# Optimization experiments

Measured on AMD Instinct MI355X. Metric: run time of the kernel, lower is better.

## Reference

```python
import jax, jax.numpy as jnp
import numpy as np

N_NODES = 50000
N_EDGES = 800000
N_GRAPHS = 256
D_IN, D_H1, D_H2, D_OUT = 64, 64, 64, 64


def gcn_conv(x, W, b, src, dst, n_nodes):
    # PyG GCNConv (eval): h = x @ W; add self-loops; deg[i] = in_deg(i) + 1;
    # out[i] = sum_{j->i} h[j] * deg[i]^-1/2 deg[j]^-1/2 + h[i]/deg[i] + b
    h = x @ W  # [N, F]
    ones = jnp.ones((src.shape[0],), dtype=x.dtype)
    deg = jax.ops.segment_sum(ones, dst, num_segments=n_nodes) + 1.0  # self loop
    dinv = jax.lax.rsqrt(deg)
    norm = dinv[src] * dinv[dst]  # [E]
    msg = h[src] * norm[:, None]  # [E, F]  (memory-bound gather)
    agg = jax.ops.segment_sum(msg, dst, num_segments=n_nodes)  # scatter-add
    agg = agg + h * (1.0 / deg)[:, None]  # self-loop contribution
    return agg + b


def setup_inputs() -> dict:
    key = jax.random.key(0)
    ks = jax.random.split(key, 12)
    x = jax.random.normal(ks[0], (N_NODES, D_IN), dtype=jnp.float32)
    src = jax.random.randint(ks[1], (N_EDGES,), 0, N_NODES)
    dst = jax.random.randint(ks[2], (N_EDGES,), 0, N_NODES)
    batch = jnp.sort(jax.random.randint(ks[3], (N_NODES,), 0, N_GRAPHS))
    def glorot(k, fin, fout):
        s = jnp.sqrt(6.0 / (fin + fout))
        return jax.random.uniform(k, (fin, fout), jnp.float32, -s, s)
    return {
        "x": x, "src": src, "dst": dst, "batch": batch,
        "W1": glorot(ks[4], D_IN, D_H1), "b1": jnp.zeros((D_H1,), jnp.float32),
        "W2": glorot(ks[5], D_H1, D_H2), "b2": jnp.zeros((D_H2,), jnp.float32),
        "W3": glorot(ks[6], D_H2, D_OUT), "b3": jnp.zeros((D_OUT,), jnp.float32),
        "Wl": glorot(ks[7], D_OUT, 1), "bl": jnp.zeros((1,), jnp.float32),
    }


def reference(x, src, dst, batch, W1, b1, W2, b2, W3, b3, Wl, bl):
    n = x.shape[0]
    h = jax.nn.relu(gcn_conv(x, W1, b1, src, dst, n))   # dropout inactive (eval)
    h = jax.nn.relu(gcn_conv(h, W2, b2, src, dst, n))
    h = jax.nn.relu(gcn_conv(h, W3, b3, src, dst, n))
    # global_mean_pool over graph ids
    sums = jax.ops.segment_sum(h, batch, num_segments=N_GRAPHS)  # [G, F]
    cnt = jax.ops.segment_sum(jnp.ones((n,), h.dtype), batch, num_segments=N_GRAPHS)
    pooled = sums / jnp.maximum(cnt, 1.0)[:, None]
    return pooled @ Wl + bl  # [G, 1]
```

## Files before the change

### kernel.cpp

```cpp
#include <hip/hip_runtime.h>

#define N_NODES 50000
#define N_EDGES 800000
#define N_GRAPHS 256
#define F 64
#define NBUCK 196
#define CAP 4608
#define P3_TILE 2048
#define P3_GRID ((N_EDGES + P3_TILE - 1) / P3_TILE)
#define BCAP 6144

__device__ __forceinline__ unsigned short f2bf(float f) {
    union { float f; unsigned u; } c; c.f = f;
    unsigned u = c.u + 0x7FFFu + ((c.u >> 16) & 1u);
    return (unsigned short)(u >> 16);
}
__device__ __forceinline__ float bfl(unsigned u) {
    union { unsigned u; float f; } c; c.u = u << 16; return c.f;
}
__device__ __forceinline__ float bfh(unsigned u) {
    union { unsigned u; float f; } c; c.u = u & 0xFFFF0000u; return c.f;
}

__global__ __launch_bounds__(256) void partition_edges(const int* __restrict__ src,
                                                       const int* __restrict__ dst,
                                                       int* __restrict__ bcur,
                                                       unsigned int* __restrict__ bpair) {
    __shared__ int bh[NBUCK], bloc[NBUCK], bpos[NBUCK];
    int t = threadIdx.x;
    int lo = blockIdx.x * P3_TILE;
    int hi = min(lo + P3_TILE, N_EDGES);
    for (int i = t; i < NBUCK; i += 256) { bh[i] = 0; bpos[i] = 0; }
    __syncthreads();
    for (int e = lo + t; e < hi; e += 256) atomicAdd(&bh[dst[e] >> 8], 1);
    __syncthreads();
    for (int i = t; i < NBUCK; i += 256)
        bloc[i] = bh[i] ? atomicAdd(&bcur[i], bh[i]) : 0;
    __syncthreads();
    for (int e = lo + t; e < hi; e += 256) {
        int d = dst[e];
        int b = d >> 8;
        int r = atomicAdd(&bpos[b], 1);
        bpair[(size_t)b * CAP + bloc[b] + r] = ((unsigned)src[e] << 8) | (unsigned)(d & 255);
    }
}

__global__ __launch_bounds__(256) void bucket_sort(const unsigned int* __restrict__ bpair,
                                                   const int* __restrict__ bcur,
                                                   int* __restrict__ eidx,
                                                   int* __restrict__ rbeg,
                                                   int* __restrict__ rend,
                                                   float* __restrict__ dinv) {
    __shared__ int cnt[256], s[256], pos[256];
    __shared__ int lout[BCAP];
    int b = blockIdx.x, t = threadIdx.x;
    int base = b * CAP;
    int sz = bcur[b];

    cnt[t] = 0;
    __syncthreads();
    for (int i = t; i < sz; i += 256) atomicAdd(&cnt[bpair[base + i] & 255], 1);
    __syncthreads();
    int v = cnt[t];
    s[t] = v;
    __syncthreads();
    for (int off = 1; off < 256; off <<= 1) {
        int u = (t >= off) ? s[t - off] : 0;
        __syncthreads();
        s[t] += u;
        __syncthreads();
    }
    int excl = s[t] - v;
    pos[t] = excl;
    int node = b * 256 + t;
    if (node < N_NODES) {
        rbeg[node] = base + excl;
        rend[node] = base + excl + v;
        dinv[node] = 1.0f / sqrtf((float)v + 1.0f);
    }
    __syncthreads();

    if (sz <= BCAP) {
        for (int i = t; i < sz; i += 256) {
            unsigned p = bpair[base + i];
            int r = atomicAdd(&pos[p & 255], 1);
            lout[r] = (int)((p >> 8) << 7);
        }
        __syncthreads();
        for (int i = t; i < sz; i += 256) eidx[base + i] = lout[i];
    } else {
        for (int i = t; i < sz; i += 256) {
            unsigned p = bpair[base + i];
            int r = atomicAdd(&pos[p & 255], 1);
            eidx[base + r] = (int)((p >> 8) << 7);
        }
    }
}

#define XSTRIDE 17
__global__ __launch_bounds__(256) void gemm64_v(const float* __restrict__ X,
                                                const float* __restrict__ W,
                                                const float* __restrict__ dinv,
                                                unsigned short* __restrict__ Hn, int n) {
    __shared__ float4 sW[64 * 16];
    __shared__ float4 sX[128 * XSTRIDE];
    int tid = threadIdx.x;
    int base = blockIdx.x * 128;

    const float4* W4 = (const float4*)W;
    for (int i = tid; i < 64 * 16; i += 256) sW[i] = W4[i];
    const float4* X4 = (const float4*)X;
    for (int i = tid; i < 128 * 16; i += 256) {
        int r = i >> 4, kg = i & 15;
        int node = base + r;
        sX[r * XSTRIDE + kg] = (node < n) ? X4[(size_t)node * 16 + kg]
                                          : make_float4(0.f, 0.f, 0.f, 0.f);
    }
    __syncthreads();

    int fg = tid & 15;
    int ng = tid >> 4;
    float4 acc[8];
#pragma unroll
    for (int ii = 0; ii < 8; ii++) acc[ii] = make_float4(0.f, 0.f, 0.f, 0.f);

    for (int kg = 0; kg < 16; kg++) {
        float4 xv[8];
#pragma unroll
        for (int ii = 0; ii < 8; ii++) xv[ii] = sX[(ng + 16 * ii) * XSTRIDE + kg];
#pragma unroll
        for (int kk = 0; kk < 4; kk++) {
            float4 wv = sW[(4 * kg + kk) * 16 + fg];
#pragma unroll
            for (int ii = 0; ii < 8; ii++) {
                float xs = (kk == 0) ? xv[ii].x : (kk == 1) ? xv[ii].y
                         : (kk == 2) ? xv[ii].z : xv[ii].w;
                acc[ii].x += wv.x * xs;
                acc[ii].y += wv.y * xs;
                acc[ii].z += wv.z * xs;
                acc[ii].w += wv.w * xs;
            }
        }
    }

    ushort4* H4 = (ushort4*)Hn;
#pragma unroll
    for (int ii = 0; ii < 8; ii++) {
        int node = base + ng + 16 * ii;
        if (node < n) {
            float d = dinv[node];
            float4 o = acc[ii];
            ushort4 u;
            u.x = f2bf(o.x * d); u.y = f2bf(o.y * d);
            u.z = f2bf(o.z * d); u.w = f2bf(o.w * d);
            H4[(size_t)node * 16 + fg] = u;
        }
    }
}

__global__ __launch_bounds__(256) void gather_layer(const int* __restrict__ rbeg,
                                                    const int* __restrict__ rend,
                                                    const int* __restrict__ eidx,
                                                    const float* __restrict__ dinv,
                                                    const unsigned short* __restrict__ Hn,
                                                    const float* __restrict__ b,
                                                    float* __restrict__ OUT, int n) {
    int w = (blockIdx.x * blockDim.x + threadIdx.x) >> 6;
    int lane = threadIdx.x & 63;
    if (w >= n) return;
    int g = lane >> 3;
    int f = lane & 7;
    int beg = rbeg[w], end = rend[w];
    const char* Hb = (const char*)Hn;

    float a0 = 0.f, a1 = 0.f, a2 = 0.f, a3 = 0.f;
    float a4 = 0.f, a5 = 0.f, a6 = 0.f, a7 = 0.f;
    int k = beg + g;
    for (; k + 8 < end; k += 16) {
        int o1 = eidx[k];
        int o2 = eidx[k + 8];
        uint4 p = *(const uint4*)(Hb + o1 + f * 16);
        uint4 q = *(const uint4*)(Hb + o2 + f * 16);
        a0 += bfl(p.x) + bfl(q.x); a1 += bfh(p.x) + bfh(q.x);
        a2 += bfl(p.y) + bfl(q.y); a3 += bfh(p.y) + bfh(q.y);
        a4 += bfl(p.z) + bfl(q.z); a5 += bfh(p.z) + bfh(q.z);
        a6 += bfl(p.w) + bfl(q.w); a7 += bfh(p.w) + bfh(q.w);
    }
    if (k < end) {
        int o1 = eidx[k];
        uint4 p = *(const uint4*)(Hb + o1 + f * 16);
        a0 += bfl(p.x); a1 += bfh(p.x);
        a2 += bfl(p.y); a3 += bfh(p.y);
        a4 += bfl(p.z); a5 += bfh(p.z);
        a6 += bfl(p.w); a7 += bfh(p.w);
    }
#pragma unroll
    for (int m = 8; m <= 32; m <<= 1) {
        a0 += __shfl_xor(a0, m); a1 += __shfl_xor(a1, m);
        a2 += __shfl_xor(a2, m); a3 += __shfl_xor(a3, m);
        a4 += __shfl_xor(a4, m); a5 += __shfl_xor(a5, m);
        a6 += __shfl_xor(a6, m); a7 += __shfl_xor(a7, m);
    }

    if (g == 0) {
        float di = dinv[w];
        uint4 hs = *(const uint4*)(Hb + (size_t)w * 128 + f * 16);
        float4 b0 = ((const float4*)b)[2 * f];
        float4 b1 = ((const float4*)b)[2 * f + 1];
        float4 o0, o1v;
        o0.x  = fmaxf(di * (a0 + bfl(hs.x)) + b0.x, 0.f);
        o0.y  = fmaxf(di * (a1 + bfh(hs.x)) + b0.y, 0.f);
        o0.z  = fmaxf(di * (a2 + bfl(hs.y)) + b0.z, 0.f);
        o0.w  = fmaxf(di * (a3 + bfh(hs.y)) + b0.w, 0.f);
        o1v.x = fmaxf(di * (a4 + bfl(hs.z)) + b1.x, 0.f);
        o1v.y = fmaxf(di * (a5 + bfh(hs.z)) + b1.y, 0.f);
        o1v.z = fmaxf(di * (a6 + bfl(hs.w)) + b1.z, 0.f);
        o1v.w = fmaxf(di * (a7 + bfh(hs.w)) + b1.w, 0.f);
        ((float4*)OUT)[(size_t)w * 16 + 2 * f]     = o0;
        ((float4*)OUT)[(size_t)w * 16 + 2 * f + 1] = o1v;
    }
}

__global__ __launch_bounds__(256) void gather_pool(const int* __restrict__ rbeg,
                                                   const int* __restrict__ rend,
                                                   const int* __restrict__ eidx,
                                                   const float* __restrict__ dinv,
                                                   const unsigned short* __restrict__ Hn,
                                                   const float* __restrict__ b,
                                                   const float* __restrict__ Wl,
                                                   float* __restrict__ pdot, int n) {
    int w = (blockIdx.x * blockDim.x + threadIdx.x) >> 6;
    int lane = threadIdx.x & 63;
    if (w >= n) return;
    int g = lane >> 3;
    int f = lane & 7;
    int beg = rbeg[w], end = rend[w];
    const char* Hb = (const char*)Hn;

    float a0 = 0.f, a1 = 0.f, a2 = 0.f, a3 = 0.f;
    float a4 = 0.f, a5 = 0.f, a6 = 0.f, a7 = 0.f;
    int k = beg + g;
    for (; k + 8 < end; k += 16) {
        int o1 = eidx[k];
        int o2 = eidx[k + 8];
        uint4 p = *(const uint4*)(Hb + o1 + f * 16);
        uint4 q = *(const uint4*)(Hb + o2 + f * 16);
        a0 += bfl(p.x) + bfl(q.x); a1 += bfh(p.x) + bfh(q.x);
        a2 += bfl(p.y) + bfl(q.y); a3 += bfh(p.y) + bfh(q.y);
        a4 += bfl(p.z) + bfl(q.z); a5 += bfh(p.z) + bfh(q.z);
        a6 += bfl(p.w) + bfl(q.w); a7 += bfh(p.w) + bfh(q.w);
    }
    if (k < end) {
        int o1 = eidx[k];
        uint4 p = *(const uint4*)(Hb + o1 + f * 16);
        a0 += bfl(p.x); a1 += bfh(p.x);
        a2 += bfl(p.y); a3 += bfh(p.y);
        a4 += bfl(p.z); a5 += bfh(p.z);
        a6 += bfl(p.w); a7 += bfh(p.w);
    }
#pragma unroll
    for (int m = 8; m <= 32; m <<= 1) {
        a0 += __shfl_xor(a0, m); a1 += __shfl_xor(a1, m);
        a2 += __shfl_xor(a2, m); a3 += __shfl_xor(a3, m);
        a4 += __shfl_xor(a4, m); a5 += __shfl_xor(a5, m);
        a6 += __shfl_xor(a6, m); a7 += __shfl_xor(a7, m);
    }

    float di = dinv[w];
    uint4 hs = *(const uint4*)(Hb + (size_t)w * 128 + f * 16);
    float4 b0 = ((const float4*)b)[2 * f];
    float4 b1 = ((const float4*)b)[2 * f + 1];
    float4 w0 = ((const float4*)Wl)[2 * f];
    float4 w1 = ((const float4*)Wl)[2 * f + 1];
    float d = 0.f;
    d += fmaxf(di * (a0 + bfl(hs.x)) + b0.x, 0.f) * w0.x;
    d += fmaxf(di * (a1 + bfh(hs.x)) + b0.y, 0.f) * w0.y;
    d += fmaxf(di * (a2 + bfl(hs.y)) + b0.z, 0.f) * w0.z;
    d += fmaxf(di * (a3 + bfh(hs.y)) + b0.w, 0.f) * w0.w;
    d += fmaxf(di * (a4 + bfl(hs.z)) + b1.x, 0.f) * w1.x;
    d += fmaxf(di * (a5 + bfh(hs.z)) + b1.y, 0.f) * w1.y;
    d += fmaxf(di * (a6 + bfl(hs.w)) + b1.z, 0.f) * w1.z;
    d += fmaxf(di * (a7 + bfh(hs.w)) + b1.w, 0.f) * w1.w;
#pragma unroll
    for (int m = 1; m <= 4; m <<= 1) d += __shfl_xor(d, m);
    if (lane == 0) pdot[w] = d;
}

__global__ __launch_bounds__(64) void final_out(const float* __restrict__ pdot,
                                                const int* __restrict__ batch,
                                                const float* __restrict__ bl,
                                                float* __restrict__ out) {
    int g = blockIdx.x;
    __shared__ int slo, shi;
    int lane = threadIdx.x;
    if (lane == 0) {
        int a = 0, b = N_NODES;
        while (a < b) { int m = (a + b) >> 1; if (batch[m] < g) a = m + 1; else b = m; }
        slo = a;
        b = N_NODES;
        while (a < b) { int m = (a + b) >> 1; if (batch[m] < g + 1) a = m + 1; else b = m; }
        shi = a;
    }
    __syncthreads();
    int lo = slo, hi = shi;
    float acc = 0.f;
    for (int i = lo + lane; i < hi; i += 64) acc += pdot[i];
#pragma unroll
    for (int off = 32; off > 0; off >>= 1) acc += __shfl_down(acc, off);
    if (lane == 0) {
        float cnt = (float)(hi - lo);
        out[g] = acc / fmaxf(cnt, 1.0f) + bl[0];
    }
}

extern "C" void kernel_launch(void* const* d_in, const int* in_sizes, int n_in,
                              void* d_out, int out_size, void* d_ws, size_t ws_size,
                              hipStream_t stream) {
    const float* x     = (const float*)d_in[0];
    const int*   src   = (const int*)d_in[1];
    const int*   dst   = (const int*)d_in[2];
    const int*   batch = (const int*)d_in[3];
    const float* W1 = (const float*)d_in[4];  const float* b1 = (const float*)d_in[5];
    const float* W2 = (const float*)d_in[6];  const float* b2 = (const float*)d_in[7];
    const float* W3 = (const float*)d_in[8];  const float* b3 = (const float*)d_in[9];
    const float* Wl = (const float*)d_in[10]; const float* bl = (const float*)d_in[11];
    float* out = (float*)d_out;

    char* ws = (char*)d_ws;
    unsigned short* Abf = (unsigned short*)ws;
    float* B       = (float*)(ws + (size_t)N_NODES * F * 2);
    float* dinv    = B + (size_t)N_NODES * F;
    float* pdot    = dinv + N_NODES;
    int*   rbeg    = (int*)(pdot + N_NODES);
    int*   rend    = rbeg + N_NODES;
    int*   bcur    = rend + N_NODES;
    unsigned int* bpair = (unsigned int*)(bcur + NBUCK);
    int*   eidx    = (int*)(bpair + (size_t)NBUCK * CAP);

    const int GEMM_GRID     = (N_NODES + 127) / 128;
    const int NODEWAVE_GRID = (N_NODES * 64 + 255) / 256;

    hipMemsetAsync(bcur, 0, NBUCK * sizeof(int), stream);
    partition_edges<<<P3_GRID, 256, 0, stream>>>(src, dst, bcur, bpair);
    bucket_sort<<<NBUCK, 256, 0, stream>>>(bpair, bcur, eidx, rbeg, rend, dinv);

    gemm64_v<<<GEMM_GRID, 256, 0, stream>>>(x, W1, dinv, Abf, N_NODES);
    gather_layer<<<NODEWAVE_GRID, 256, 0, stream>>>(rbeg, rend, eidx, dinv, Abf, b1, B, N_NODES);

    gemm64_v<<<GEMM_GRID, 256, 0, stream>>>(B, W2, dinv, Abf, N_NODES);
    gather_layer<<<NODEWAVE_GRID, 256, 0, stream>>>(rbeg, rend, eidx, dinv, Abf, b2, B, N_NODES);

    gemm64_v<<<GEMM_GRID, 256, 0, stream>>>(B, W3, dinv, Abf, N_NODES);
    gather_pool<<<NODEWAVE_GRID, 256, 0, stream>>>(rbeg, rend, eidx, dinv, Abf, b3, Wl, pdot, N_NODES);

    final_out<<<N_GRAPHS, 64, 0, stream>>>(pdot, batch, bl, out);
}
```

Measured before the change: 234.6 us.

## Store layer activations in bf16 and gather 8 nodes per wave

```diff
diff --git a/kernel.cpp b/kernel.cpp
--- a/kernel.cpp
+++ b/kernel.cpp
@@ -14,6 +14,9 @@
     union { float f; unsigned u; } c; c.f = f;
     unsigned u = c.u + 0x7FFFu + ((c.u >> 16) & 1u);
     return (unsigned short)(u >> 16);
+}
+__device__ __forceinline__ unsigned pack2bf(float lo, float hi) {
+    return (unsigned)f2bf(lo) | ((unsigned)f2bf(hi) << 16);
 }
 __device__ __forceinline__ float bfl(unsigned u) {
     union { unsigned u; float f; } c; c.u = u << 16; return c.f;
@@ -98,7 +101,8 @@
 }
 
 #define XSTRIDE 17
-__global__ __launch_bounds__(256) void gemm64_v(const float* __restrict__ X,
+template <bool BF16IN>
+__global__ __launch_bounds__(256) void gemm64_t(const void* __restrict__ Xv,
                                                 const float* __restrict__ W,
                                                 const float* __restrict__ dinv,
                                                 unsigned short* __restrict__ Hn, int n) {
@@ -109,12 +113,24 @@
 
     const float4* W4 = (const float4*)W;
     for (int i = tid; i < 64 * 16; i += 256) sW[i] = W4[i];
-    const float4* X4 = (const float4*)X;
-    for (int i = tid; i < 128 * 16; i += 256) {
-        int r = i >> 4, kg = i & 15;
-        int node = base + r;
-        sX[r * XSTRIDE + kg] = (node < n) ? X4[(size_t)node * 16 + kg]
-                                          : make_float4(0.f, 0.f, 0.f, 0.f);
+    if (BF16IN) {
+        const uint4* X4 = (const uint4*)Xv;
+        for (int i = tid; i < 128 * 8; i += 256) {
+            int r = i >> 3, c = i & 7;
+            int node = base + r;
+            uint4 u = (node < n) ? X4[(size_t)node * 8 + c]
+                                 : make_uint4(0u, 0u, 0u, 0u);
+            sX[r * XSTRIDE + 2 * c]     = make_float4(bfl(u.x), bfh(u.x), bfl(u.y), bfh(u.y));
+            sX[r * XSTRIDE + 2 * c + 1] = make_float4(bfl(u.z), bfh(u.z), bfl(u.w), bfh(u.w));
+        }
+    } else {
+        const float4* X4 = (const float4*)Xv;
+        for (int i = tid; i < 128 * 16; i += 256) {
+            int r = i >> 4, kg = i & 15;
+            int node = base + r;
+            sX[r * XSTRIDE + kg] = (node < n) ? X4[(size_t)node * 16 + kg]
+                                              : make_float4(0.f, 0.f, 0.f, 0.f);
+        }
     }
     __syncthreads();
 
@@ -164,21 +180,22 @@
                                                     const float* __restrict__ dinv,
                                                     const unsigned short* __restrict__ Hn,
                                                     const float* __restrict__ b,
-                                                    float* __restrict__ OUT, int n) {
-    int w = (blockIdx.x * blockDim.x + threadIdx.x) >> 6;
+                                                    unsigned short* __restrict__ OUT, int n) {
+    int wv = (blockIdx.x * blockDim.x + threadIdx.x) >> 6;
     int lane = threadIdx.x & 63;
-    if (w >= n) return;
-    int g = lane >> 3;
-    int f = lane & 7;
-    int beg = rbeg[w], end = rend[w];
+    int ns = lane >> 3, f = lane & 7;
+    int node = wv * 8 + ns;
+    bool valid = node < n;
+    int beg = valid ? rbeg[node] : 0;
+    int end = valid ? rend[node] : 0;
     const char* Hb = (const char*)Hn;
 
     float a0 = 0.f, a1 = 0.f, a2 = 0.f, a3 = 0.f;
     float a4 = 0.f, a5 = 0.f, a6 = 0.f, a7 = 0.f;
-    int k = beg + g;
-    for (; k + 8 < end; k += 16) {
+    int k = beg;
+    for (; k + 1 < end; k += 2) {
         int o1 = eidx[k];
-        int o2 = eidx[k + 8];
+        int o2 = eidx[k + 1];
         uint4 p = *(const uint4*)(Hb + o1 + f * 16);
         uint4 q = *(const uint4*)(Hb + o2 + f * 16);
         a0 += bfl(p.x) + bfl(q.x); a1 += bfh(p.x) + bfh(q.x);
@@ -194,30 +211,24 @@
         a4 += bfl(p.z); a5 += bfh(p.z);
         a6 += bfl(p.w); a7 += bfh(p.w);
     }
-#pragma unroll
-    for (int m = 8; m <= 32; m <<= 1) {
-        a0 += __shfl_xor(a0, m); a1 += __shfl_xor(a1, m);
-        a2 += __shfl_xor(a2, m); a3 += __shfl_xor(a3, m);
-        a4 += __shfl_xor(a4, m); a5 += __shfl_xor(a5, m);
-        a6 += __shfl_xor(a6, m); a7 += __shfl_xor(a7, m);
-    }
-
-    if (g == 0) {
-        float di = dinv[w];
-        uint4 hs = *(const uint4*)(Hb + (size_t)w * 128 + f * 16);
+
+    if (valid) {
+        float di = dinv[node];
+        uint4 hs = *(const uint4*)(Hb + (size_t)node * 128 + f * 16);
         float4 b0 = ((const float4*)b)[2 * f];
         float4 b1 = ((const float4*)b)[2 * f + 1];
-        float4 o0, o1v;
-        o0.x  = fmaxf(di * (a0 + bfl(hs.x)) + b0.x, 0.f);
-        o0.y  = fmaxf(di * (a1 + bfh(hs.x)) + b0.y, 0.f);
-        o0.z  = fmaxf(di * (a2 + bfl(hs.y)) + b0.z, 0.f);
-        o0.w  = fmaxf(di * (a3 + bfh(hs.y)) + b0.w, 0.f);
-        o1v.x = fmaxf(di * (a4 + bfl(hs.z)) + b1.x, 0.f);
-        o1v.y = fmaxf(di * (a5 + bfh(hs.z)) + b1.y, 0.f);
-        o1v.z = fmaxf(di * (a6 + bfl(hs.w)) + b1.z, 0.f);
-        o1v.w = fmaxf(di * (a7 + bfh(hs.w)) + b1.w, 0.f);
-        ((float4*)OUT)[(size_t)w * 16 + 2 * f]     = o0;
-        ((float4*)OUT)[(size_t)w * 16 + 2 * f + 1] = o1v;
+        float v0 = fmaxf(di * (a0 + bfl(hs.x)) + b0.x, 0.f);
+        float v1 = fmaxf(di * (a1 + bfh(hs.x)) + b0.y, 0.f);
+        float v2 = fmaxf(di * (a2 + bfl(hs.y)) + b0.z, 0.f);
+        float v3 = fmaxf(di * (a3 + bfh(hs.y)) + b0.w, 0.f);
+        float v4 = fmaxf(di * (a4 + bfl(hs.z)) + b1.x, 0.f);
+        float v5 = fmaxf(di * (a5 + bfh(hs.z)) + b1.y, 0.f);
+        float v6 = fmaxf(di * (a6 + bfl(hs.w)) + b1.z, 0.f);
+        float v7 = fmaxf(di * (a7 + bfh(hs.w)) + b1.w, 0.f);
+        uint4 u;
+        u.x = pack2bf(v0, v1); u.y = pack2bf(v2, v3);
+        u.z = pack2bf(v4, v5); u.w = pack2bf(v6, v7);
+        ((uint4*)OUT)[(size_t)node * 8 + f] = u;
     }
 }
 
@@ -229,20 +240,21 @@
                                                    const float* __restrict__ b,
                                                    const float* __restrict__ Wl,
                                                    float* __restrict__ pdot, int n) {
-    int w = (blockIdx.x * blockDim.x + threadIdx.x) >> 6;
+    int wv = (blockIdx.x * blockDim.x + threadIdx.x) >> 6;
     int lane = threadIdx.x & 63;
-    if (w >= n) return;
-    int g = lane >> 3;
-    int f = lane & 7;
-    int beg = rbeg[w], end = rend[w];
+    int ns = lane >> 3, f = lane & 7;
+    int node = wv * 8 + ns;
+    bool valid = node < n;
+    int beg = valid ? rbeg[node] : 0;
+    int end = valid ? rend[node] : 0;
     const char* Hb = (const char*)Hn;
 
     float a0 = 0.f, a1 = 0.f, a2 = 0.f, a3 = 0.f;
     float a4 = 0.f, a5 = 0.f, a6 = 0.f, a7 = 0.f;
-    int k = beg + g;
-    for (; k + 8 < end; k += 16) {
+    int k = beg;
+    for (; k + 1 < end; k += 2) {
         int o1 = eidx[k];
-        int o2 = eidx[k + 8];
+        int o2 = eidx[k + 1];
         uint4 p = *(const uint4*)(Hb + o1 + f * 16);
         uint4 q = *(const uint4*)(Hb + o2 + f * 16);
         a0 += bfl(p.x) + bfl(q.x); a1 += bfh(p.x) + bfh(q.x);
@@ -258,16 +270,10 @@
         a4 += bfl(p.z); a5 += bfh(p.z);
         a6 += bfl(p.w); a7 += bfh(p.w);
     }
-#pragma unroll
-    for (int m = 8; m <= 32; m <<= 1) {
-        a0 += __shfl_xor(a0, m); a1 += __shfl_xor(a1, m);
-        a2 += __shfl_xor(a2, m); a3 += __shfl_xor(a3, m);
-        a4 += __shfl_xor(a4, m); a5 += __shfl_xor(a5, m);
-        a6 += __shfl_xor(a6, m); a7 += __shfl_xor(a7, m);
-    }
-
-    float di = dinv[w];
-    uint4 hs = *(const uint4*)(Hb + (size_t)w * 128 + f * 16);
+
+    float di = valid ? dinv[node] : 0.f;
+    uint4 hs = valid ? *(const uint4*)(Hb + (size_t)node * 128 + f * 16)
+                     : make_uint4(0u, 0u, 0u, 0u);
     float4 b0 = ((const float4*)b)[2 * f];
     float4 b1 = ((const float4*)b)[2 * f + 1];
     float4 w0 = ((const float4*)Wl)[2 * f];
@@ -283,7 +289,7 @@
     d += fmaxf(di * (a7 + bfh(hs.w)) + b1.w, 0.f) * w1.w;
 #pragma unroll
     for (int m = 1; m <= 4; m <<= 1) d += __shfl_xor(d, m);
-    if (lane == 0) pdot[w] = d;
+    if (valid && f == 0) pdot[node] = d;
 }
 
 __global__ __launch_bounds__(64) void final_out(const float* __restrict__ pdot,
@@ -328,8 +334,8 @@
 
     char* ws = (char*)d_ws;
     unsigned short* Abf = (unsigned short*)ws;
-    float* B       = (float*)(ws + (size_t)N_NODES * F * 2);
-    float* dinv    = B + (size_t)N_NODES * F;
+    unsigned short* Bbf = Abf + (size_t)N_NODES * F;
+    float* dinv    = (float*)(Bbf + (size_t)N_NODES * F);
     float* pdot    = dinv + N_NODES;
     int*   rbeg    = (int*)(pdot + N_NODES);
     int*   rend    = rbeg + N_NODES;
@@ -337,21 +343,21 @@
     unsigned int* bpair = (unsigned int*)(bcur + NBUCK);
     int*   eidx    = (int*)(bpair + (size_t)NBUCK * CAP);
 
-    const int GEMM_GRID     = (N_NODES + 127) / 128;
-    const int NODEWAVE_GRID = (N_NODES * 64 + 255) / 256;
+    const int GEMM_GRID   = (N_NODES + 127) / 128;
+    const int GATHER_GRID = (N_NODES + 31) / 32;
 
     hipMemsetAsync(bcur, 0, NBUCK * sizeof(int), stream);
     partition_edges<<<P3_GRID, 256, 0, stream>>>(src, dst, bcur, bpair);
     bucket_sort<<<NBUCK, 256, 0, stream>>>(bpair, bcur, eidx, rbeg, rend, dinv);
 
-    gemm64_v<<<GEMM_GRID, 256, 0, stream>>>(x, W1, dinv, Abf, N_NODES);
-    gather_layer<<<NODEWAVE_GRID, 256, 0, stream>>>(rbeg, rend, eidx, dinv, Abf, b1, B, N_NODES);
-
-    gemm64_v<<<GEMM_GRID, 256, 0, stream>>>(B, W2, dinv, Abf, N_NODES);
-    gather_layer<<<NODEWAVE_GRID, 256, 0, stream>>>(rbeg, rend, eidx, dinv, Abf, b2, B, N_NODES);
-
-    gemm64_v<<<GEMM_GRID, 256, 0, stream>>>(B, W3, dinv, Abf, N_NODES);
-    gather_pool<<<NODEWAVE_GRID, 256, 0, stream>>>(rbeg, rend, eidx, dinv, Abf, b3, Wl, pdot, N_NODES);
+    gemm64_t<false><<<GEMM_GRID, 256, 0, stream>>>((const void*)x, W1, dinv, Abf, N_NODES);
+    gather_layer<<<GATHER_GRID, 256, 0, stream>>>(rbeg, rend, eidx, dinv, Abf, b1, Bbf, N_NODES);
+
+    gemm64_t<true><<<GEMM_GRID, 256, 0, stream>>>((const void*)Bbf, W2, dinv, Abf, N_NODES);
+    gather_layer<<<GATHER_GRID, 256, 0, stream>>>(rbeg, rend, eidx, dinv, Abf, b2, Bbf, N_NODES);
+
+    gemm64_t<true><<<GEMM_GRID, 256, 0, stream>>>((const void*)Bbf, W3, dinv, Abf, N_NODES);
+    gather_pool<<<GATHER_GRID, 256, 0, stream>>>(rbeg, rend, eidx, dinv, Abf, b3, Wl, pdot, N_NODES);
 
     final_out<<<N_GRAPHS, 64, 0, stream>>>(pdot, batch, bl, out);
 }
```

New measurement: 221.9 us. -5.4%, faster.
